# Kernel tuning notes

Hardware: AMD Instinct MI355X
Metric: run time of the kernel (lower is better)

Reference implementation:

```python
import jax, jax.numpy as jnp
from jax import lax
import numpy as np

B, T, C = 32, 1024, 512
K = 3
MAX_DUR = 4            # durations drawn from [0,5) -> max value 4
L_MAX = T * MAX_DUR    # static padded mel length (torch pads to batch max; we pad to static max)
EPS = 1e-5


def conv_ln_block(x, w, b, g, beta):
    # x: [B,T,C]; torch ConvLNBlock: permute -> Conv1d(SAME) -> relu -> permute -> LayerNorm -> dropout(eval=id)
    y = lax.conv_general_dilated(x.transpose(0, 2, 1), w, (1,), 'SAME',
                                 dimension_numbers=('NCH', 'OIH', 'NCH')) + b[None, :, None]
    y = jax.nn.relu(y).transpose(0, 2, 1)  # [B,T,Cout]
    mu = y.mean(-1, keepdims=True)
    var = y.var(-1, keepdims=True)
    return (y - mu) * lax.rsqrt(var + EPS) * g + beta


def regulate(batch, durations, token_lengths):
    # Vectorized equivalent of DurationRegulator.inflate: repeat token t durations[b,t] times,
    # concatenate, pad. Implemented as cumsum + searchsorted gather (single pass, no ragged loops).
    pos = jnp.arange(T)
    valid = pos[None, :] < token_lengths[:, None]          # [B,T]
    d = jnp.where(valid, durations, 0)
    total = d.sum(axis=1)
    # torch: if durs.sum()==0 -> fill with 1
    d = jnp.where((total == 0)[:, None], valid.astype(d.dtype), d)
    total = d.sum(axis=1)                                   # [B]
    cum = jnp.cumsum(d, axis=1)                             # inclusive cumsum [B,T]
    frames = jnp.arange(L_MAX)
    idx = jax.vmap(lambda c: jnp.searchsorted(c, frames, side='right'))(cum)  # [B,L_MAX]
    idx = jnp.clip(idx, 0, T - 1)
    out = jnp.take_along_axis(batch, idx[:, :, None], axis=1)                 # [B,L_MAX,C]
    frame_mask = frames[None, :] < total[:, None]
    out = out * frame_mask[:, :, None].astype(batch.dtype)
    return out, total.astype(jnp.float32)


def setup_inputs() -> dict:
    key = jax.random.key(0)
    ks = jax.random.split(key, 8)
    batch = jax.random.normal(ks[0], (B, T, C), dtype=jnp.float32)
    token_lengths = jax.random.randint(ks[1], (B,), T // 2, T + 1).astype(jnp.int32)
    mask = jnp.arange(T)[None, :] < token_lengths[:, None]
    label_durations = jax.random.randint(ks[2], (B, T), 0, MAX_DUR + 1).astype(jnp.int32)
    s1 = 1.0 / np.sqrt(C * K)
    s2 = 1.0 / np.sqrt(C * K)
    params = {
        'conv1_w': jax.random.uniform(ks[3], (C, C, K), minval=-s1, maxval=s1, dtype=jnp.float32),
        'conv1_b': jnp.zeros((C,), jnp.float32),
        'ln1_g': jnp.ones((C,), jnp.float32), 'ln1_b': jnp.zeros((C,), jnp.float32),
        'conv2_w': jax.random.uniform(ks[4], (C, C, K), minval=-s2, maxval=s2, dtype=jnp.float32),
        'conv2_b': jnp.zeros((C,), jnp.float32),
        'ln2_g': jnp.ones((C,), jnp.float32), 'ln2_b': jnp.zeros((C,), jnp.float32),
        'lin_w': jax.random.uniform(ks[5], (C, 1), minval=-1/np.sqrt(C), maxval=1/np.sqrt(C), dtype=jnp.float32),
        'lin_b': jnp.zeros((1,), jnp.float32),
    }
    return dict(batch=batch, token_lengths=token_lengths, mask=mask,
                label_durations=label_durations, **params)


def reference(batch, token_lengths, mask, label_durations,
              conv1_w, conv1_b, ln1_g, ln1_b,
              conv2_w, conv2_b, ln2_g, ln2_b,
              lin_w, lin_b):
    # VariancePredictor: two ConvLN blocks + Linear(out_channels, 1), masked fill 0
    h = conv_ln_block(batch, conv1_w, conv1_b, ln1_g, ln1_b)
    h = conv_ln_block(h, conv2_w, conv2_b, ln2_g, ln2_b)
    predicted_durations = h @ lin_w + lin_b                      # [B,T,1]
    predicted_durations = jnp.where(mask[:, :, None], predicted_durations, 0.0)
    # label_durations provided -> regulator uses labels (training path), alpha=1
    padded_batch, mel_lengths = regulate(batch, label_durations, token_lengths)
    return padded_batch, mel_lengths, predicted_durations
```

## Files before the change

### kernel.cpp

```cpp
#include <hip/hip_runtime.h>
#include <hip/hip_bf16.h>
#include <stdint.h>


typedef _Float16 f16;
typedef _Float16 f16x8 __attribute__((ext_vector_type(8)));
typedef float f32x4 __attribute__((ext_vector_type(4)));

#define B_    32
#define T_    1024
#define TP_   1026
#define C_    512
#define LMAX_ 4096
#define KDIM  1536

#define XPAD_OFF   0u
#define H1PAD_OFF  33619968u
#define W1T_OFF    67239936u
#define W2T_OFF    68812800u
#define TOT_OFF    137494528u
#define IDX_OFF    137495040u

#define AS1C(p) ((const __attribute__((address_space(1))) void*)(p))
#define AS3(p)  ((__attribute__((address_space(3))) void*)(p))

__global__ __launch_bounds__(256) void prep_pad(const float* __restrict__ batch,
                                                f16* __restrict__ xpad,
                                                f16* __restrict__ h1pad) {
    int row = blockIdx.x * 4 + (threadIdx.x >> 6);
    int lane = threadIdx.x & 63;
    int b = row / TP_, tt = row % TP_;
    size_t dsto = (size_t)row * C_ + lane * 8;
    if (tt == 0 || tt == TP_ - 1) {
        f16x8 z = {};
        *(f16x8*)(xpad + dsto) = z;
        *(f16x8*)(h1pad + dsto) = z;
    } else {
        const float* src = batch + ((size_t)(b * T_ + tt - 1)) * C_ + lane * 8;
        float4 v0 = ((const float4*)src)[0];
        float4 v1 = ((const float4*)src)[1];
        f16x8 h;
        h[0] = (f16)v0.x; h[1] = (f16)v0.y; h[2] = (f16)v0.z; h[3] = (f16)v0.w;
        h[4] = (f16)v1.x; h[5] = (f16)v1.y; h[6] = (f16)v1.z; h[7] = (f16)v1.w;
        *(f16x8*)(xpad + dsto) = h;
    }
}

__global__ __launch_bounds__(256) void prep_w(const float* __restrict__ w1,
                                              const float* __restrict__ w2,
                                              f16* __restrict__ w1t,
                                              f16* __restrict__ w2t) {
    int o = blockIdx.x;
    const float* w = blockIdx.y ? w2 : w1;
    f16* wt = blockIdx.y ? w2t : w1t;
    for (int j = threadIdx.x; j < KDIM; j += 256) {
        int tap = j >> 9, i = j & 511;
        wt[(size_t)o * KDIM + j] = (f16)w[(size_t)o * KDIM + i * 3 + tap];
    }
}

__global__ __launch_bounds__(1024) void scan_kernel(const int* __restrict__ dur,
                                                    const int* __restrict__ tlen,
                                                    int* __restrict__ idxarr,
                                                    int* __restrict__ total,
                                                    float* __restrict__ mel_out) {
    int b = blockIdx.x, t = threadIdx.x;
    __shared__ int sd[1024];
    __shared__ int sv[1024];
    int L = tlen[b];
    int valid = (t < L) ? 1 : 0;
    int d = valid ? dur[b * T_ + t] : 0;
    sd[t] = d; sv[t] = valid;
    __syncthreads();
    for (int off = 1; off < 1024; off <<= 1) {
        int x = 0, y = 0;
        if (t >= off) { x = sd[t - off]; y = sv[t - off]; }
        __syncthreads();
        sd[t] += x; sv[t] += y;
        __syncthreads();
    }
    int totd = sd[1023];
    int cur  = (totd == 0) ? sv[t] : sd[t];
    int prev = (t == 0) ? 0 : ((totd == 0) ? sv[t - 1] : sd[t - 1]);
    for (int f = prev; f < cur; f++) idxarr[b * LMAX_ + f] = t;
    if (t == 1023) {
        int tt = (totd == 0) ? sv[1023] : totd;
        total[b] = tt;
        mel_out[b] = (float)tt;
    }
}

template<int EPI>
__global__ __launch_bounds__(256, 2) void gemm_fused(const f16* __restrict__ A,
                                                     const f16* __restrict__ Bw,
                                                     const float* __restrict__ bias,
                                                     const float* __restrict__ g,
                                                     const float* __restrict__ be,
                                                     const float* __restrict__ lw,
                                                     const float* __restrict__ lb,
                                                     const int* __restrict__ tlen,
                                                     f16* __restrict__ hpad,
                                                     float* __restrict__ pred) {
    __shared__ f16 As[64 * 64];
    __shared__ f16 Bs[512 * 64];
    __shared__ float red[4][64][2];
    const int tid = threadIdx.x;
    const int lane = tid & 63;
    const int w = tid >> 6;
    const int m0 = blockIdx.x * 64;
    const int arow0 = (m0 >> 10) * TP_ + (m0 & 1023);
    const int wn = w * 128;

    f32x4 acc[4][8];
#pragma unroll
    for (int i = 0; i < 4; i++)
#pragma unroll
        for (int j = 0; j < 8; j++) acc[i][j] = (f32x4){0.f, 0.f, 0.f, 0.f};

    const int lrow = lane >> 3;
    const int gran = (lane & 7) ^ lrow;
    const f16* aB = A + (size_t)(arow0 + lrow) * C_ + gran * 8;
    const f16* bB = Bw + (size_t)lrow * KDIM + gran * 8;

    for (int kk = 0; kk < KDIM; kk += 64) {
        __syncthreads();
#pragma unroll
        for (int i = 0; i < 2; i++) {
            const int rb = (w + i * 4) * 8;
            __builtin_amdgcn_global_load_lds(AS1C(aB + (size_t)rb * C_ + kk),
                                             AS3(&As[rb * 64]), 16, 0, 0);
        }
#pragma unroll
        for (int j = 0; j < 16; j++) {
            const int rb = (w + j * 4) * 8;
            __builtin_amdgcn_global_load_lds(AS1C(bB + (size_t)rb * KDIM + kk),
                                             AS3(&Bs[rb * 64]), 16, 0, 0);
        }
        __syncthreads();
#pragma unroll
        for (int ks = 0; ks < 2; ks++) {
            const int sl = ((ks << 2) + (lane >> 4)) ^ (lane & 7);
            f16x8 af[4], bf[8];
#pragma unroll
            for (int mi = 0; mi < 4; mi++)
                af[mi] = *(const f16x8*)&As[(mi * 16 + (lane & 15)) * 64 + sl * 8];
#pragma unroll
            for (int ni = 0; ni < 8; ni++)
                bf[ni] = *(const f16x8*)&Bs[(wn + ni * 16 + (lane & 15)) * 64 + sl * 8];
#pragma unroll
            for (int mi = 0; mi < 4; mi++)
#pragma unroll
                for (int ni = 0; ni < 8; ni++)
                    acc[mi][ni] = __builtin_amdgcn_mfma_f32_16x16x32_f16(
                        af[mi], bf[ni], acc[mi][ni], 0, 0, 0);
        }
    }

    const int col = lane & 15;
    const int row4 = (lane >> 4) * 4;

    float bn[8];
#pragma unroll
    for (int ni = 0; ni < 8; ni++) bn[ni] = bias[wn + ni * 16 + col];
    float s_[4][4], q_[4][4];
#pragma unroll
    for (int mi = 0; mi < 4; mi++)
#pragma unroll
        for (int r = 0; r < 4; r++) { s_[mi][r] = 0.f; q_[mi][r] = 0.f; }
#pragma unroll
    for (int mi = 0; mi < 4; mi++)
#pragma unroll
        for (int ni = 0; ni < 8; ni++)
#pragma unroll
            for (int r = 0; r < 4; r++) {
                float v = acc[mi][ni][r] + bn[ni];
                v = v > 0.f ? v : 0.f;
                acc[mi][ni][r] = v;
                s_[mi][r] += v;
                q_[mi][r] += v * v;
            }
#pragma unroll
    for (int m = 8; m; m >>= 1)
#pragma unroll
        for (int mi = 0; mi < 4; mi++)
#pragma unroll
            for (int r = 0; r < 4; r++) {
                s_[mi][r] += __shfl_xor(s_[mi][r], m, 64);
                q_[mi][r] += __shfl_xor(q_[mi][r], m, 64);
            }
    if (col == 0) {
#pragma unroll
        for (int mi = 0; mi < 4; mi++)
#pragma unroll
            for (int r = 0; r < 4; r++) {
                int row = mi * 16 + row4 + r;
                red[w][row][0] = s_[mi][r];
                red[w][row][1] = q_[mi][r];
            }
    }
    __syncthreads();
    float mu_[4][4], rs_[4][4];
#pragma unroll
    for (int mi = 0; mi < 4; mi++)
#pragma unroll
        for (int r = 0; r < 4; r++) {
            int row = mi * 16 + row4 + r;
            float S = red[0][row][0] + red[1][row][0] + red[2][row][0] + red[3][row][0];
            float Q = red[0][row][1] + red[1][row][1] + red[2][row][1] + red[3][row][1];
            float mu = S * (1.f / 512.f);
            float x = Q * (1.f / 512.f) - mu * mu + 1e-5f;
            float rs = rsqrtf(x);
            rs = rs * (1.5f - 0.5f * x * rs * rs);
            mu_[mi][r] = mu; rs_[mi][r] = rs;
        }

    if (EPI == 0) {
        const int bb = m0 >> 10, t0 = m0 & 1023;
        f16* hbase = hpad + ((size_t)(bb * TP_ + t0 + 1)) * C_;
#pragma unroll
        for (int ni = 0; ni < 8; ni++) {
            int n = wn + ni * 16 + col;
            float gv = g[n], ev = be[n];
#pragma unroll
            for (int mi = 0; mi < 4; mi++)
#pragma unroll
                for (int r = 0; r < 4; r++) {
                    int lm = mi * 16 + row4 + r;
                    float v = (acc[mi][ni][r] - mu_[mi][r]) * rs_[mi][r] * gv + ev;
                    hbase[(size_t)lm * C_ + n] = (f16)v;
                }
        }
    } else {
        float p_[4][4];
#pragma unroll
        for (int mi = 0; mi < 4; mi++)
#pragma unroll
            for (int r = 0; r < 4; r++) p_[mi][r] = 0.f;
#pragma unroll
        for (int ni = 0; ni < 8; ni++) {
            int n = wn + ni * 16 + col;
            float gv = g[n], ev = be[n], wv = lw[n];
#pragma unroll
            for (int mi = 0; mi < 4; mi++)
#pragma unroll
                for (int r = 0; r < 4; r++)
                    p_[mi][r] += ((acc[mi][ni][r] - mu_[mi][r]) * rs_[mi][r] * gv + ev) * wv;
        }
#pragma unroll
        for (int m = 8; m; m >>= 1)
#pragma unroll
            for (int mi = 0; mi < 4; mi++)
#pragma unroll
                for (int r = 0; r < 4; r++)
                    p_[mi][r] += __shfl_xor(p_[mi][r], m, 64);
        __syncthreads();
        if (col == 0) {
#pragma unroll
            for (int mi = 0; mi < 4; mi++)
#pragma unroll
                for (int r = 0; r < 4; r++)
                    red[w][mi * 16 + row4 + r][0] = p_[mi][r];
        }
        __syncthreads();
        if (tid < 64) {
            int m = m0 + tid;
            float p = red[0][tid][0] + red[1][tid][0] + red[2][tid][0] + red[3][tid][0];
            int bb = m >> 10, t = m & 1023;
            pred[m] = (t < tlen[bb]) ? (p + lb[0]) : 0.f;
        }
    }
}

__global__ __launch_bounds__(256) void gather_kernel(const float* __restrict__ batch,
                                                     const int* __restrict__ idxarr,
                                                     const int* __restrict__ total,
                                                     float* __restrict__ out) {
    int gw = blockIdx.x * 4 + (threadIdx.x >> 6);
    int lane = threadIdx.x & 63;
    int b = gw >> 12;
    int l = gw & (LMAX_ - 1);
    int tot = total[b];
    float4* dst = (float4*)(out + ((size_t)b * LMAX_ + l) * C_);
    if (l < tot) {
        int idx = idxarr[gw];
        const float4* src = (const float4*)(batch + ((size_t)b * T_ + idx) * C_);
        dst[lane] = src[lane];
        dst[lane + 64] = src[lane + 64];
    } else {
        float4 z = {0.f, 0.f, 0.f, 0.f};
        dst[lane] = z;
        dst[lane + 64] = z;
    }
}

extern "C" void kernel_launch(void* const* d_in, const int* in_sizes, int n_in,
                              void* d_out, int out_size, void* d_ws, size_t ws_size,
                              hipStream_t stream) {
    const float* batch = (const float*)d_in[0];
    const int* tlen    = (const int*)d_in[1];
    const int* durs    = (const int*)d_in[3];
    const float* w1  = (const float*)d_in[4];
    const float* b1  = (const float*)d_in[5];
    const float* g1  = (const float*)d_in[6];
    const float* be1 = (const float*)d_in[7];
    const float* w2  = (const float*)d_in[8];
    const float* b2  = (const float*)d_in[9];
    const float* g2  = (const float*)d_in[10];
    const float* be2 = (const float*)d_in[11];
    const float* lw  = (const float*)d_in[12];
    const float* lb  = (const float*)d_in[13];

    float* out      = (float*)d_out;
    float* mel_out  = out + (size_t)B_ * LMAX_ * C_;
    float* pred_out = mel_out + B_;

    char* ws    = (char*)d_ws;
    f16* xpad   = (f16*)(ws + XPAD_OFF);
    f16* h1pad  = (f16*)(ws + H1PAD_OFF);
    f16* w1t    = (f16*)(ws + W1T_OFF);
    f16* w2t    = (f16*)(ws + W2T_OFF);
    int* tot    = (int*)(ws + TOT_OFF);
    int* idxarr = (int*)(ws + IDX_OFF);

    prep_pad<<<B_ * TP_ / 4, 256, 0, stream>>>(batch, xpad, h1pad);
    prep_w<<<dim3(512, 2), 256, 0, stream>>>(w1, w2, w1t, w2t);
    scan_kernel<<<B_, 1024, 0, stream>>>(durs, tlen, idxarr, tot, mel_out);
    gemm_fused<0><<<512, 256, 0, stream>>>(xpad, w1t, b1, g1, be1,
                                           nullptr, nullptr, nullptr, h1pad, nullptr);
    gemm_fused<1><<<512, 256, 0, stream>>>(h1pad, w2t, b2, g2, be2,
                                           lw, lb, tlen, nullptr, pred_out);
    gather_kernel<<<B_ * LMAX_ / 4, 256, 0, stream>>>(batch, idxarr, tot, out);
}
```

Baseline: 498.1 us.

## Double-buffer GEMM LDS stages and enlarge block tile to 128 rows

The fused conv-as-GEMM kernels now use 512-thread blocks covering 128 output rows, with each wave computing a 64x128 sub-tile. The K loop takes 32-wide steps and double-buffers the A and B tiles in LDS, so the next stage's global-to-LDS loads are issued before the current stage's MFMAs and only one barrier is needed per step. The aim is to hide load latency and halve how often the weight tile is reloaded per output row. In exchange the grid shrinks to 256 blocks, which may underfill the GPU's compute units, and the LDS reduction buffer is aliased onto the tile buffers.

```diff
diff --git a/kernel.cpp b/kernel.cpp
--- a/kernel.cpp
+++ b/kernel.cpp
@@ -13,6 +13,7 @@
 #define C_    512
 #define LMAX_ 4096
 #define KDIM  1536
+#define NK    48
 
 #define XPAD_OFF   0u
 #define H1PAD_OFF  33619968u
@@ -91,7 +92,7 @@
 }
 
 template<int EPI>
-__global__ __launch_bounds__(256, 2) void gemm_fused(const f16* __restrict__ A,
+__global__ __launch_bounds__(512, 2) void gemm_fused(const f16* __restrict__ A,
                                                      const f16* __restrict__ Bw,
                                                      const float* __restrict__ bias,
                                                      const float* __restrict__ g,
@@ -101,15 +102,20 @@
                                                      const int* __restrict__ tlen,
                                                      f16* __restrict__ hpad,
                                                      float* __restrict__ pred) {
-    __shared__ f16 As[64 * 64];
-    __shared__ f16 Bs[512 * 64];
-    __shared__ float red[4][64][2];
+    __shared__ f16 lds_[40960];
+    f16* const A0 = lds_;
+    f16* const A1 = lds_ + 4096;
+    f16* const B0 = lds_ + 8192;
+    f16* const B1 = lds_ + 24576;
+    float* red = (float*)lds_;
+
     const int tid = threadIdx.x;
     const int lane = tid & 63;
     const int w = tid >> 6;
-    const int m0 = blockIdx.x * 64;
+    const int wm = (w & 1) * 64;
+    const int wn = (w >> 1) * 128;
+    const int m0 = blockIdx.x * 128;
     const int arow0 = (m0 >> 10) * TP_ + (m0 & 1023);
-    const int wn = w * 128;
 
     f32x4 acc[4][8];
 #pragma unroll
@@ -117,47 +123,51 @@
 #pragma unroll
         for (int j = 0; j < 8; j++) acc[i][j] = (f32x4){0.f, 0.f, 0.f, 0.f};
 
-    const int lrow = lane >> 3;
-    const int gran = (lane & 7) ^ lrow;
-    const f16* aB = A + (size_t)(arow0 + lrow) * C_ + gran * 8;
-    const f16* bB = Bw + (size_t)lrow * KDIM + gran * 8;
-
-    for (int kk = 0; kk < KDIM; kk += 64) {
-        __syncthreads();
-#pragma unroll
-        for (int i = 0; i < 2; i++) {
-            const int rb = (w + i * 4) * 8;
-            __builtin_amdgcn_global_load_lds(AS1C(aB + (size_t)rb * C_ + kk),
-                                             AS3(&As[rb * 64]), 16, 0, 0);
-        }
-#pragma unroll
-        for (int j = 0; j < 16; j++) {
-            const int rb = (w + j * 4) * 8;
-            __builtin_amdgcn_global_load_lds(AS1C(bB + (size_t)rb * KDIM + kk),
-                                             AS3(&Bs[rb * 64]), 16, 0, 0);
-        }
-        __syncthreads();
-#pragma unroll
-        for (int ks = 0; ks < 2; ks++) {
-            const int sl = ((ks << 2) + (lane >> 4)) ^ (lane & 7);
-            f16x8 af[4], bf[8];
-#pragma unroll
-            for (int mi = 0; mi < 4; mi++)
-                af[mi] = *(const f16x8*)&As[(mi * 16 + (lane & 15)) * 64 + sl * 8];
+    const int perm = (lane & 3) ^ ((lane >> 2) & 3) ^ ((lane >> 4) & 3);
+    const f16* aB = A + (size_t)(arow0 + w * 16 + (lane >> 2)) * C_ + perm * 8;
+    const f16* bB = Bw + (size_t)(w * 16 + (lane >> 2)) * KDIM + perm * 8;
+
+#define STAGE(Ad, Bd, kofs) do {                                              \
+        __builtin_amdgcn_global_load_lds(AS1C(aB + (kofs)),                   \
+                                         AS3((Ad) + w * 512), 16, 0, 0);      \
+        _Pragma("unroll")                                                     \
+        for (int j_ = 0; j_ < 4; j_++) {                                      \
+            __builtin_amdgcn_global_load_lds(                                 \
+                AS1C(bB + (size_t)(128 * j_) * KDIM + (kofs)),                \
+                AS3((Bd) + (w + 8 * j_) * 512), 16, 0, 0);                    \
+        }                                                                     \
+    } while (0)
+
+    STAGE(A0, B0, 0);
+    __syncthreads();
+
+    f16 *Ac = A0, *An = A1, *Bc = B0, *Bn = B1;
+    for (int t = 0; t < NK; ++t) {
+        if (t + 1 < NK) STAGE(An, Bn, (t + 1) * 32);
+        const int base = perm * 8;
+        f16x8 af[4], bf[8];
+#pragma unroll
+        for (int mi = 0; mi < 4; mi++)
+            af[mi] = *(const f16x8*)&Ac[(wm + mi * 16 + (lane & 15)) * 32 + base];
+#pragma unroll
+        for (int ni = 0; ni < 8; ni++)
+            bf[ni] = *(const f16x8*)&Bc[(wn + ni * 16 + (lane & 15)) * 32 + base];
+#pragma unroll
+        for (int mi = 0; mi < 4; mi++)
 #pragma unroll
             for (int ni = 0; ni < 8; ni++)
-                bf[ni] = *(const f16x8*)&Bs[(wn + ni * 16 + (lane & 15)) * 64 + sl * 8];
-#pragma unroll
-            for (int mi = 0; mi < 4; mi++)
-#pragma unroll
-                for (int ni = 0; ni < 8; ni++)
-                    acc[mi][ni] = __builtin_amdgcn_mfma_f32_16x16x32_f16(
-                        af[mi], bf[ni], acc[mi][ni], 0, 0, 0);
-        }
-    }
+                acc[mi][ni] = __builtin_amdgcn_mfma_f32_16x16x32_f16(
+                    af[mi], bf[ni], acc[mi][ni], 0, 0, 0);
+        __syncthreads();
+        f16* tp;
+        tp = Ac; Ac = An; An = tp;
+        tp = Bc; Bc = Bn; Bn = tp;
+    }
+#undef STAGE
 
     const int col = lane & 15;
     const int row4 = (lane >> 4) * 4;
+    const int nw = w >> 1;
 
     float bn[8];
 #pragma unroll
@@ -193,9 +203,9 @@
         for (int mi = 0; mi < 4; mi++)
 #pragma unroll
             for (int r = 0; r < 4; r++) {
-                int row = mi * 16 + row4 + r;
-                red[w][row][0] = s_[mi][r];
-                red[w][row][1] = q_[mi][r];
+                int row = wm + mi * 16 + row4 + r;
+                red[(nw * 128 + row) * 2]     = s_[mi][r];
+                red[(nw * 128 + row) * 2 + 1] = q_[mi][r];
             }
     }
     __syncthreads();
@@ -204,9 +214,11 @@
     for (int mi = 0; mi < 4; mi++)
 #pragma unroll
         for (int r = 0; r < 4; r++) {
-            int row = mi * 16 + row4 + r;
-            float S = red[0][row][0] + red[1][row][0] + red[2][row][0] + red[3][row][0];
-            float Q = red[0][row][1] + red[1][row][1] + red[2][row][1] + red[3][row][1];
+            int row = wm + mi * 16 + row4 + r;
+            float S = red[row * 2]             + red[(128 + row) * 2]
+                    + red[(256 + row) * 2]     + red[(384 + row) * 2];
+            float Q = red[row * 2 + 1]         + red[(128 + row) * 2 + 1]
+                    + red[(256 + row) * 2 + 1] + red[(384 + row) * 2 + 1];
             float mu = S * (1.f / 512.f);
             float x = Q * (1.f / 512.f) - mu * mu + 1e-5f;
             float rs = rsqrtf(x);
@@ -225,7 +237,7 @@
             for (int mi = 0; mi < 4; mi++)
 #pragma unroll
                 for (int r = 0; r < 4; r++) {
-                    int lm = mi * 16 + row4 + r;
+                    int lm = wm + mi * 16 + row4 + r;
                     float v = (acc[mi][ni][r] - mu_[mi][r]) * rs_[mi][r] * gv + ev;
                     hbase[(size_t)lm * C_ + n] = (f16)v;
                 }
@@ -259,12 +271,12 @@
             for (int mi = 0; mi < 4; mi++)
 #pragma unroll
                 for (int r = 0; r < 4; r++)
-                    red[w][mi * 16 + row4 + r][0] = p_[mi][r];
-        }
-        __syncthreads();
-        if (tid < 64) {
+                    red[nw * 128 + wm + mi * 16 + row4 + r] = p_[mi][r];
+        }
+        __syncthreads();
+        if (tid < 128) {
             int m = m0 + tid;
-            float p = red[0][tid][0] + red[1][tid][0] + red[2][tid][0] + red[3][tid][0];
+            float p = red[tid] + red[128 + tid] + red[256 + tid] + red[384 + tid];
             int bb = m >> 10, t = m & 1023;
             pred[m] = (t < tlen[bb]) ? (p + lb[0]) : 0.f;
         }
@@ -325,9 +337,9 @@
     prep_pad<<<B_ * TP_ / 4, 256, 0, stream>>>(batch, xpad, h1pad);
     prep_w<<<dim3(512, 2), 256, 0, stream>>>(w1, w2, w1t, w2t);
     scan_kernel<<<B_, 1024, 0, stream>>>(durs, tlen, idxarr, tot, mel_out);
-    gemm_fused<0><<<512, 256, 0, stream>>>(xpad, w1t, b1, g1, be1,
+    gemm_fused<0><<<256, 512, 0, stream>>>(xpad, w1t, b1, g1, be1,
                                            nullptr, nullptr, nullptr, h1pad, nullptr);
-    gemm_fused<1><<<512, 256, 0, stream>>>(h1pad, w2t, b2, g2, be2,
+    gemm_fused<1><<<256, 512, 0, stream>>>(h1pad, w2t, b2, g2, be2,
                                            lw, lb, tlen, nullptr, pred_out);
     gather_kernel<<<B_ * LMAX_ / 4, 256, 0, stream>>>(batch, idxarr, tot, out);
 }
```

Measured after the change: 503.3 us. About the same (+1.0%).

## Split GEMM tiles across N and move LayerNorm to separate kernels

Applied to the files above, without the earlier changes.

Each conv GEMM now uses 128x256 output tiles over a 2D grid instead of 64x512 full-row tiles, which cuts how often the weight matrix is reloaded per output row. Because a block no longer holds a whole row, the first LayerNorm moves into its own kernel that reads an f16 intermediate. The second block's LayerNorm plus linear head is folded algebraically into per-row partial sums (sum, sum of squares, gamma*w dot) that a small finalize kernel combines. This adds two launches and an extra round trip of the intermediate through memory.

```diff
diff --git a/kernel.cpp b/kernel.cpp
--- a/kernel.cpp
+++ b/kernel.cpp
@@ -18,8 +18,12 @@
 #define H1PAD_OFF  33619968u
 #define W1T_OFF    67239936u
 #define W2T_OFF    68812800u
+#define YWS_OFF    70385664u
 #define TOT_OFF    137494528u
 #define IDX_OFF    137495040u
+#define GWL_OFF    138019328u
+#define K12_OFF    138021376u
+#define STAT2_OFF  138021888u
 
 #define AS1C(p) ((const __attribute__((address_space(1))) void*)(p))
 #define AS3(p)  ((__attribute__((address_space(3))) void*)(p))
@@ -49,13 +53,42 @@
 __global__ __launch_bounds__(256) void prep_w(const float* __restrict__ w1,
                                               const float* __restrict__ w2,
                                               f16* __restrict__ w1t,
-                                              f16* __restrict__ w2t) {
+                                              f16* __restrict__ w2t,
+                                              const float* __restrict__ g2,
+                                              const float* __restrict__ be2,
+                                              const float* __restrict__ lw,
+                                              float* __restrict__ gwl,
+                                              float* __restrict__ k12) {
     int o = blockIdx.x;
     const float* w = blockIdx.y ? w2 : w1;
     f16* wt = blockIdx.y ? w2t : w1t;
     for (int j = threadIdx.x; j < KDIM; j += 256) {
         int tap = j >> 9, i = j & 511;
         wt[(size_t)o * KDIM + j] = (f16)w[(size_t)o * KDIM + i * 3 + tap];
+    }
+    if (blockIdx.x == 0 && blockIdx.y == 0) {
+        __shared__ float rk[4][2];
+        float k1 = 0.f, k2 = 0.f;
+        for (int c = threadIdx.x; c < C_; c += 256) {
+            float gw_ = g2[c] * lw[c];
+            gwl[c] = gw_;
+            k1 += gw_;
+            k2 += be2[c] * lw[c];
+        }
+#pragma unroll
+        for (int m = 32; m; m >>= 1) {
+            k1 += __shfl_xor(k1, m, 64);
+            k2 += __shfl_xor(k2, m, 64);
+        }
+        if ((threadIdx.x & 63) == 0) {
+            rk[threadIdx.x >> 6][0] = k1;
+            rk[threadIdx.x >> 6][1] = k2;
+        }
+        __syncthreads();
+        if (threadIdx.x == 0) {
+            k12[0] = rk[0][0] + rk[1][0] + rk[2][0] + rk[3][0];
+            k12[1] = rk[0][1] + rk[1][1] + rk[2][1] + rk[3][1];
+        }
     }
 }
 
@@ -91,25 +124,22 @@
 }
 
 template<int EPI>
-__global__ __launch_bounds__(256, 2) void gemm_fused(const f16* __restrict__ A,
-                                                     const f16* __restrict__ Bw,
-                                                     const float* __restrict__ bias,
-                                                     const float* __restrict__ g,
-                                                     const float* __restrict__ be,
-                                                     const float* __restrict__ lw,
-                                                     const float* __restrict__ lb,
-                                                     const int* __restrict__ tlen,
-                                                     f16* __restrict__ hpad,
-                                                     float* __restrict__ pred) {
-    __shared__ f16 As[64 * 64];
-    __shared__ f16 Bs[512 * 64];
-    __shared__ float red[4][64][2];
+__global__ __launch_bounds__(256, 2) void gemm_k(const f16* __restrict__ A,
+                                                 const f16* __restrict__ Bw,
+                                                 const float* __restrict__ bias,
+                                                 f16* __restrict__ Y,
+                                                 const float* __restrict__ gwl,
+                                                 float4* __restrict__ stats) {
+    __shared__ f16 As[128 * 64];
+    __shared__ f16 Bs[256 * 64];
     const int tid = threadIdx.x;
     const int lane = tid & 63;
     const int w = tid >> 6;
-    const int m0 = blockIdx.x * 64;
+    const int m0 = blockIdx.x * 128;
+    const int n0 = blockIdx.y * 256;
     const int arow0 = (m0 >> 10) * TP_ + (m0 & 1023);
-    const int wn = w * 128;
+    const int wm = (w & 1) * 64;
+    const int wn = (w >> 1) * 128;
 
     f32x4 acc[4][8];
 #pragma unroll
@@ -120,18 +150,18 @@
     const int lrow = lane >> 3;
     const int gran = (lane & 7) ^ lrow;
     const f16* aB = A + (size_t)(arow0 + lrow) * C_ + gran * 8;
-    const f16* bB = Bw + (size_t)lrow * KDIM + gran * 8;
+    const f16* bB = Bw + (size_t)(n0 + lrow) * KDIM + gran * 8;
 
     for (int kk = 0; kk < KDIM; kk += 64) {
         __syncthreads();
 #pragma unroll
-        for (int i = 0; i < 2; i++) {
+        for (int i = 0; i < 4; i++) {
             const int rb = (w + i * 4) * 8;
             __builtin_amdgcn_global_load_lds(AS1C(aB + (size_t)rb * C_ + kk),
                                              AS3(&As[rb * 64]), 16, 0, 0);
         }
 #pragma unroll
-        for (int j = 0; j < 16; j++) {
+        for (int j = 0; j < 8; j++) {
             const int rb = (w + j * 4) * 8;
             __builtin_amdgcn_global_load_lds(AS1C(bB + (size_t)rb * KDIM + kk),
                                              AS3(&Bs[rb * 64]), 16, 0, 0);
@@ -143,7 +173,7 @@
             f16x8 af[4], bf[8];
 #pragma unroll
             for (int mi = 0; mi < 4; mi++)
-                af[mi] = *(const f16x8*)&As[(mi * 16 + (lane & 15)) * 64 + sl * 8];
+                af[mi] = *(const f16x8*)&As[(wm + mi * 16 + (lane & 15)) * 64 + sl * 8];
 #pragma unroll
             for (int ni = 0; ni < 8; ni++)
                 bf[ni] = *(const f16x8*)&Bs[(wn + ni * 16 + (lane & 15)) * 64 + sl * 8];
@@ -159,116 +189,130 @@
     const int col = lane & 15;
     const int row4 = (lane >> 4) * 4;
 
-    float bn[8];
-#pragma unroll
-    for (int ni = 0; ni < 8; ni++) bn[ni] = bias[wn + ni * 16 + col];
-    float s_[4][4], q_[4][4];
-#pragma unroll
-    for (int mi = 0; mi < 4; mi++)
-#pragma unroll
-        for (int r = 0; r < 4; r++) { s_[mi][r] = 0.f; q_[mi][r] = 0.f; }
-#pragma unroll
-    for (int mi = 0; mi < 4; mi++)
-#pragma unroll
-        for (int ni = 0; ni < 8; ni++)
-#pragma unroll
-            for (int r = 0; r < 4; r++) {
-                float v = acc[mi][ni][r] + bn[ni];
-                v = v > 0.f ? v : 0.f;
-                acc[mi][ni][r] = v;
-                s_[mi][r] += v;
-                q_[mi][r] += v * v;
+    if (EPI == 0) {
+#pragma unroll
+        for (int ni = 0; ni < 8; ni++) {
+            int n = n0 + wn + ni * 16 + col;
+            float bn = bias[n];
+#pragma unroll
+            for (int mi = 0; mi < 4; mi++) {
+#pragma unroll
+                for (int r = 0; r < 4; r++) {
+                    int m = m0 + wm + mi * 16 + row4 + r;
+                    float v = acc[mi][ni][r] + bn;
+                    Y[(size_t)m * C_ + n] = (f16)(v > 0.f ? v : 0.f);
+                }
             }
-#pragma unroll
-    for (int m = 8; m; m >>= 1)
+        }
+    } else {
+        float bn[8], gw[8];
+#pragma unroll
+        for (int ni = 0; ni < 8; ni++) {
+            int n = n0 + wn + ni * 16 + col;
+            bn[ni] = bias[n];
+            gw[ni] = gwl[n];
+        }
+        float s_[4][4], q_[4][4], u_[4][4];
 #pragma unroll
         for (int mi = 0; mi < 4; mi++)
 #pragma unroll
-            for (int r = 0; r < 4; r++) {
-                s_[mi][r] += __shfl_xor(s_[mi][r], m, 64);
-                q_[mi][r] += __shfl_xor(q_[mi][r], m, 64);
-            }
-    if (col == 0) {
+            for (int r = 0; r < 4; r++) { s_[mi][r] = 0.f; q_[mi][r] = 0.f; u_[mi][r] = 0.f; }
 #pragma unroll
         for (int mi = 0; mi < 4; mi++)
 #pragma unroll
-            for (int r = 0; r < 4; r++) {
-                int row = mi * 16 + row4 + r;
-                red[w][row][0] = s_[mi][r];
-                red[w][row][1] = q_[mi][r];
-            }
-    }
-    __syncthreads();
-    float mu_[4][4], rs_[4][4];
-#pragma unroll
-    for (int mi = 0; mi < 4; mi++)
-#pragma unroll
-        for (int r = 0; r < 4; r++) {
-            int row = mi * 16 + row4 + r;
-            float S = red[0][row][0] + red[1][row][0] + red[2][row][0] + red[3][row][0];
-            float Q = red[0][row][1] + red[1][row][1] + red[2][row][1] + red[3][row][1];
-            float mu = S * (1.f / 512.f);
-            float x = Q * (1.f / 512.f) - mu * mu + 1e-5f;
-            float rs = rsqrtf(x);
-            rs = rs * (1.5f - 0.5f * x * rs * rs);
-            mu_[mi][r] = mu; rs_[mi][r] = rs;
-        }
-
-    if (EPI == 0) {
-        const int bb = m0 >> 10, t0 = m0 & 1023;
-        f16* hbase = hpad + ((size_t)(bb * TP_ + t0 + 1)) * C_;
-#pragma unroll
-        for (int ni = 0; ni < 8; ni++) {
-            int n = wn + ni * 16 + col;
-            float gv = g[n], ev = be[n];
+            for (int ni = 0; ni < 8; ni++)
+#pragma unroll
+                for (int r = 0; r < 4; r++) {
+                    float v = acc[mi][ni][r] + bn[ni];
+                    v = v > 0.f ? v : 0.f;
+                    s_[mi][r] += v;
+                    q_[mi][r] += v * v;
+                    u_[mi][r] += v * gw[ni];
+                }
+#pragma unroll
+        for (int m = 8; m; m >>= 1)
 #pragma unroll
             for (int mi = 0; mi < 4; mi++)
 #pragma unroll
                 for (int r = 0; r < 4; r++) {
-                    int lm = mi * 16 + row4 + r;
-                    float v = (acc[mi][ni][r] - mu_[mi][r]) * rs_[mi][r] * gv + ev;
-                    hbase[(size_t)lm * C_ + n] = (f16)v;
+                    s_[mi][r] += __shfl_xor(s_[mi][r], m, 64);
+                    q_[mi][r] += __shfl_xor(q_[mi][r], m, 64);
+                    u_[mi][r] += __shfl_xor(u_[mi][r], m, 64);
                 }
-        }
-    } else {
-        float p_[4][4];
-#pragma unroll
-        for (int mi = 0; mi < 4; mi++)
-#pragma unroll
-            for (int r = 0; r < 4; r++) p_[mi][r] = 0.f;
-#pragma unroll
-        for (int ni = 0; ni < 8; ni++) {
-            int n = wn + ni * 16 + col;
-            float gv = g[n], ev = be[n], wv = lw[n];
+        __syncthreads();
+        float* red = (float*)As;
+        if (col == 0) {
 #pragma unroll
             for (int mi = 0; mi < 4; mi++)
 #pragma unroll
-                for (int r = 0; r < 4; r++)
-                    p_[mi][r] += ((acc[mi][ni][r] - mu_[mi][r]) * rs_[mi][r] * gv + ev) * wv;
-        }
-#pragma unroll
-        for (int m = 8; m; m >>= 1)
-#pragma unroll
-            for (int mi = 0; mi < 4; mi++)
-#pragma unroll
-                for (int r = 0; r < 4; r++)
-                    p_[mi][r] += __shfl_xor(p_[mi][r], m, 64);
-        __syncthreads();
-        if (col == 0) {
-#pragma unroll
-            for (int mi = 0; mi < 4; mi++)
-#pragma unroll
-                for (int r = 0; r < 4; r++)
-                    red[w][mi * 16 + row4 + r][0] = p_[mi][r];
-        }
-        __syncthreads();
-        if (tid < 64) {
-            int m = m0 + tid;
-            float p = red[0][tid][0] + red[1][tid][0] + red[2][tid][0] + red[3][tid][0];
-            int bb = m >> 10, t = m & 1023;
-            pred[m] = (t < tlen[bb]) ? (p + lb[0]) : 0.f;
-        }
-    }
+                for (int r = 0; r < 4; r++) {
+                    int row = wm + mi * 16 + row4 + r;
+                    int idx = ((w >> 1) * 128 + row) * 3;
+                    red[idx]     = s_[mi][r];
+                    red[idx + 1] = q_[mi][r];
+                    red[idx + 2] = u_[mi][r];
+                }
+        }
+        __syncthreads();
+        if (tid < 128) {
+            float S = red[tid * 3]     + red[(128 + tid) * 3];
+            float Q = red[tid * 3 + 1] + red[(128 + tid) * 3 + 1];
+            float U = red[tid * 3 + 2] + red[(128 + tid) * 3 + 2];
+            stats[(size_t)(m0 + tid) * 2 + blockIdx.y] = (float4){S, Q, U, 0.f};
+        }
+    }
+}
+
+__global__ __launch_bounds__(256) void ln_kernel(const f16* __restrict__ Y,
+                                                 const float* __restrict__ g,
+                                                 const float* __restrict__ be,
+                                                 f16* __restrict__ hpad) {
+    int row = blockIdx.x * 4 + (threadIdx.x >> 6);
+    int lane = threadIdx.x & 63;
+    f16x8 yv = *(const f16x8*)(Y + (size_t)row * C_ + lane * 8);
+    float v[8];
+#pragma unroll
+    for (int i = 0; i < 8; i++) v[i] = (float)yv[i];
+    float s = 0.f, q = 0.f;
+#pragma unroll
+    for (int i = 0; i < 8; i++) { s += v[i]; q += v[i] * v[i]; }
+#pragma unroll
+    for (int m = 32; m; m >>= 1) { s += __shfl_xor(s, m, 64); q += __shfl_xor(q, m, 64); }
+    float mu = s * (1.f / 512.f);
+    float x = q * (1.f / 512.f) - mu * mu + 1e-5f;
+    float rs = rsqrtf(x);
+    rs = rs * (1.5f - 0.5f * x * rs * rs);
+    const float4 g0 = ((const float4*)g)[lane * 2], g1 = ((const float4*)g)[lane * 2 + 1];
+    const float4 e0 = ((const float4*)be)[lane * 2], e1 = ((const float4*)be)[lane * 2 + 1];
+    f16x8 h;
+    h[0] = (f16)((v[0] - mu) * rs * g0.x + e0.x);
+    h[1] = (f16)((v[1] - mu) * rs * g0.y + e0.y);
+    h[2] = (f16)((v[2] - mu) * rs * g0.z + e0.z);
+    h[3] = (f16)((v[3] - mu) * rs * g0.w + e0.w);
+    h[4] = (f16)((v[4] - mu) * rs * g1.x + e1.x);
+    h[5] = (f16)((v[5] - mu) * rs * g1.y + e1.y);
+    h[6] = (f16)((v[6] - mu) * rs * g1.z + e1.z);
+    h[7] = (f16)((v[7] - mu) * rs * g1.w + e1.w);
+    int b = row >> 10, t = row & 1023;
+    *(f16x8*)(hpad + ((size_t)(b * TP_ + t + 1)) * C_ + lane * 8) = h;
+}
+
+__global__ __launch_bounds__(256) void finalize2(const float4* __restrict__ stats,
+                                                 const float* __restrict__ k12,
+                                                 const float* __restrict__ lb,
+                                                 const int* __restrict__ tlen,
+                                                 float* __restrict__ pred) {
+    int m = blockIdx.x * 256 + threadIdx.x;
+    float4 a = stats[(size_t)m * 2];
+    float4 b = stats[(size_t)m * 2 + 1];
+    float S = a.x + b.x, Q = a.y + b.y, U = a.z + b.z;
+    float mu = S * (1.f / 512.f);
+    float x = Q * (1.f / 512.f) - mu * mu + 1e-5f;
+    float rs = rsqrtf(x);
+    rs = rs * (1.5f - 0.5f * x * rs * rs);
+    float p = rs * (U - mu * k12[0]) + k12[1] + lb[0];
+    int bb = m >> 10, t = m & 1023;
+    pred[m] = (t < tlen[bb]) ? p : 0.f;
 }
 
 __global__ __launch_bounds__(256) void gather_kernel(const float* __restrict__ batch,
@@ -319,15 +363,19 @@
     f16* h1pad  = (f16*)(ws + H1PAD_OFF);
     f16* w1t    = (f16*)(ws + W1T_OFF);
     f16* w2t    = (f16*)(ws + W2T_OFF);
+    f16* yws    = (f16*)(ws + YWS_OFF);
     int* tot    = (int*)(ws + TOT_OFF);
     int* idxarr = (int*)(ws + IDX_OFF);
+    float* gwl  = (float*)(ws + GWL_OFF);
+    float* k12  = (float*)(ws + K12_OFF);
+    float4* st2 = (float4*)(ws + STAT2_OFF);
 
     prep_pad<<<B_ * TP_ / 4, 256, 0, stream>>>(batch, xpad, h1pad);
-    prep_w<<<dim3(512, 2), 256, 0, stream>>>(w1, w2, w1t, w2t);
+    prep_w<<<dim3(512, 2), 256, 0, stream>>>(w1, w2, w1t, w2t, g2, be2, lw, gwl, k12);
     scan_kernel<<<B_, 1024, 0, stream>>>(durs, tlen, idxarr, tot, mel_out);
-    gemm_fused<0><<<512, 256, 0, stream>>>(xpad, w1t, b1, g1, be1,
-                                           nullptr, nullptr, nullptr, h1pad, nullptr);
-    gemm_fused<1><<<512, 256, 0, stream>>>(h1pad, w2t, b2, g2, be2,
-                                           lw, lb, tlen, nullptr, pred_out);
+    gemm_k<0><<<dim3(256, 2), 256, 0, stream>>>(xpad, w1t, b1, yws, nullptr, nullptr);
+    ln_kernel<<<8192, 256, 0, stream>>>(yws, g1, be1, h1pad);
+    gemm_k<1><<<dim3(256, 2), 256, 0, stream>>>(h1pad, w2t, b2, nullptr, gwl, st2);
+    finalize2<<<128, 256, 0, stream>>>(st2, k12, lb, tlen, pred_out);
     gather_kernel<<<B_ * LMAX_ / 4, 256, 0, stream>>>(batch, idxarr, tot, out);
 }
```

Result: faster. 462.1 us (-7.2%).
